# Kernel optimization log

Measured on AMD Instinct MI355X. Metric: run time of the kernel, lower is better.

Reference implementation:

```python
import jax, jax.numpy as jnp
import numpy as np

N = 100000
E = 1600000
F_IN, HID, OUT = 64, 64, 32

def setup_inputs() -> dict:
    key = jax.random.key(0)
    ks = jax.random.split(key, 16)
    s = 0.05
    return {
        "x": jax.random.normal(ks[0], (N, F_IN), jnp.float32),
        "edge_index": jax.random.randint(ks[1], (2, E), 0, N, jnp.int64),
        "edge_attr": jax.random.uniform(ks[2], (E, 1), jnp.float32),
        # distance_processor: Linear(1,16) -> ReLU -> Linear(16,1)
        "Wd1": jax.random.normal(ks[3], (1, 16), jnp.float32) * s,
        "bd1": jnp.zeros((16,), jnp.float32),
        "Wd2": jax.random.normal(ks[4], (16, 1), jnp.float32) * s,
        "bd2": jnp.zeros((1,), jnp.float32),
        # conv1 / conv2 GCN linear weights (in, out) + post-aggregation bias
        "W1c": jax.random.normal(ks[5], (F_IN, HID), jnp.float32) * s,
        "b1c": jnp.zeros((HID,), jnp.float32),
        "W2c": jax.random.normal(ks[6], (HID, HID), jnp.float32) * s,
        "b2c": jnp.zeros((HID,), jnp.float32),
        # output head Linear(hidden, output)
        "Wo": jax.random.normal(ks[7], (HID, OUT), jnp.float32) * s,
        "bo": jnp.zeros((OUT,), jnp.float32),
    }


def _gcn_conv(x, src, dst, ew, W, b, n_nodes):
    """PyG GCNConv with edge weights: add self-loops (weight 1), symmetric norm."""
    h = x @ W                                            # [N, out]
    loop = jnp.arange(n_nodes, dtype=src.dtype)
    src_a = jnp.concatenate([src, loop])                 # [E+N]
    dst_a = jnp.concatenate([dst, loop])
    ew_a = jnp.concatenate([ew, jnp.ones((n_nodes,), ew.dtype)])
    deg = jax.ops.segment_sum(ew_a, dst_a, num_segments=n_nodes)
    dinv = jnp.where(deg > 0, jax.lax.rsqrt(jnp.maximum(deg, 1e-30)), 0.0)
    norm = dinv[src_a] * ew_a * dinv[dst_a]              # [E+N]
    msg = norm[:, None] * h[src_a]                       # gather + scale
    agg = jax.ops.segment_sum(msg, dst_a, num_segments=n_nodes)  # scatter-add
    return agg + b


def reference(x, edge_index, edge_attr, Wd1, bd1, Wd2, bd2, W1c, b1c, W2c, b2c, Wo, bo):
    src, dst = edge_index[0], edge_index[1]
    # edge weight from tiny MLP on distance, squeezed to [E]
    hmlp = jax.nn.relu(edge_attr @ Wd1 + bd1)
    ew = jax.nn.sigmoid(hmlp @ Wd2 + bd2)[:, 0]
    h = jax.nn.relu(_gcn_conv(x, src, dst, ew, W1c, b1c, N))
    # dropout is identity in eval mode
    h = _gcn_conv(h, src, dst, ew, W2c, b2c, N)
    return h @ Wo + bo
```

## Files before the change

### kernel.cpp

```cpp
#include <hip/hip_runtime.h>
#include <math.h>

#define NBMAX 400

__device__ inline ushort f2bf(float f) {
    unsigned u = __float_as_uint(f);
    u += 0x7fff + ((u >> 16) & 1);
    return (ushort)(u >> 16);
}
__device__ inline float bf2f(ushort u) {
    return __uint_as_float(((unsigned)u) << 16);
}

__global__ __launch_bounds__(256) void k_tobf16(const float4* __restrict__ X4,
                                                ushort4* __restrict__ Y4, int n4) {
    int i = blockIdx.x * 256 + threadIdx.x;
    if (i >= n4) return;
    float4 v = X4[i];
    ushort4 o;
    o.x = f2bf(v.x); o.y = f2bf(v.y); o.z = f2bf(v.z); o.w = f2bf(v.w);
    Y4[i] = o;
}

__global__ __launch_bounds__(256) void k_edge3(const float* __restrict__ ea,
                                               const float* __restrict__ Wd1,
                                               const float* __restrict__ bd1,
                                               const float* __restrict__ Wd2,
                                               const float* __restrict__ bd2,
                                               const int* __restrict__ dstv,
                                               float* __restrict__ ew,
                                               int* __restrict__ bcnt,
                                               int E, int chunk) {
    __shared__ float w1[16], b1[16], w2[16];
    __shared__ float b2s;
    __shared__ int lh[NBMAX];
    int tid = threadIdx.x;
    if (tid < 16) {
        w1[tid] = Wd1[tid];
        b1[tid] = bd1[tid];
        w2[tid] = Wd2[tid];
    }
    if (tid == 0) b2s = bd2[0];
    for (int i = tid; i < NBMAX; i += 256) lh[i] = 0;
    __syncthreads();
    int start = blockIdx.x * chunk;
    int end = min(E, start + chunk);
    for (int e = start + tid; e < end; e += 256) {
        float a = ea[e];
        float s = b2s;
#pragma unroll
        for (int j = 0; j < 16; ++j) {
            float h = fmaxf(a * w1[j] + b1[j], 0.0f);
            s += h * w2[j];
        }
        ew[e] = 1.0f / (1.0f + expf(-s));
        atomicAdd(&lh[dstv[e] >> 8], 1);
    }
    __syncthreads();
    for (int i = tid; i < NBMAX; i += 256)
        if (lh[i]) atomicAdd(&bcnt[i], lh[i]);
}

__global__ __launch_bounds__(512) void k_scan_b(const int* __restrict__ bcnt,
                                                int* __restrict__ bbase,
                                                int* __restrict__ bcursor, int nb) {
    __shared__ int s[512];
    int t = threadIdx.x;
    int c = (t < nb) ? bcnt[t] : 0;
    s[t] = c;
    __syncthreads();
    for (int o = 1; o < 512; o <<= 1) {
        int v = (t >= o) ? s[t - o] : 0;
        __syncthreads();
        s[t] += v;
        __syncthreads();
    }
    if (t < nb) {
        int excl = s[t] - c;
        bbase[t] = excl;
        bcursor[t] = excl;
    }
}

__global__ __launch_bounds__(256) void k_scatter(const int* __restrict__ srcv,
                                                 const int* __restrict__ dstv,
                                                 const float* __restrict__ ew,
                                                 int* __restrict__ bcursor,
                                                 int* __restrict__ sdst,
                                                 int* __restrict__ ssrc,
                                                 float* __restrict__ sw,
                                                 int E, int chunk) {
    __shared__ int lh[NBMAX], gb[NBMAX], lc[NBMAX];
    int tid = threadIdx.x;
    for (int i = tid; i < NBMAX; i += 256) { lh[i] = 0; lc[i] = 0; }
    __syncthreads();
    int start = blockIdx.x * chunk;
    int end = min(E, start + chunk);
    for (int e = start + tid; e < end; e += 256)
        atomicAdd(&lh[dstv[e] >> 8], 1);
    __syncthreads();
    for (int i = tid; i < NBMAX; i += 256)
        gb[i] = lh[i] ? atomicAdd(&bcursor[i], lh[i]) : 0;
    __syncthreads();
    for (int e = start + tid; e < end; e += 256) {
        int d = dstv[e];
        int b = d >> 8;
        int p = gb[b] + atomicAdd(&lc[b], 1);
        sdst[p] = d;
        ssrc[p] = srcv[e];
        sw[p] = ew[e];
    }
}

__global__ __launch_bounds__(256) void k_group(const int* __restrict__ sdst,
                                               const int* __restrict__ ssrc,
                                               const float* __restrict__ sw,
                                               const int* __restrict__ bbase,
                                               int2* __restrict__ slots,
                                               int* __restrict__ rowst,
                                               int* __restrict__ cntg,
                                               float* __restrict__ dinv,
                                               int nb, int n, int E) {
    __shared__ int cnt[256], sc[256], ls[256], cur[256];
    __shared__ float dsum[256];
    int b = blockIdx.x;
    int tid = threadIdx.x;
    int r0 = bbase[b];
    int r1 = (b + 1 < nb) ? bbase[b + 1] : E;
    cnt[tid] = 0; cur[tid] = 0; dsum[tid] = 0.0f;
    __syncthreads();
    for (int i = r0 + tid; i < r1; i += 256) {
        int dl = sdst[i] & 255;
        atomicAdd(&cnt[dl], 1);
        atomicAdd(&dsum[dl], sw[i]);
    }
    __syncthreads();
    sc[tid] = cnt[tid];
    __syncthreads();
    for (int o = 1; o < 256; o <<= 1) {
        int v = (tid >= o) ? sc[tid - o] : 0;
        __syncthreads();
        sc[tid] += v;
        __syncthreads();
    }
    ls[tid] = sc[tid] - cnt[tid];
    int dst = (b << 8) + tid;
    if (dst < n) {
        rowst[dst] = r0 + ls[tid];
        cntg[dst] = cnt[tid];
        dinv[dst] = 1.0f / sqrtf(1.0f + dsum[tid]);
    }
    __syncthreads();
    for (int i = r0 + tid; i < r1; i += 256) {
        int dl = sdst[i] & 255;
        int p = r0 + ls[dl] + atomicAdd(&cur[dl], 1);
        slots[p] = make_int2(ssrc[i], __float_as_int(sw[i]));
    }
}

__global__ __launch_bounds__(256) void k_edge2(const float* __restrict__ ea,
                                               const float* __restrict__ Wd1,
                                               const float* __restrict__ bd1,
                                               const float* __restrict__ Wd2,
                                               const float* __restrict__ bd2,
                                               const int* __restrict__ dstv,
                                               float* __restrict__ ew,
                                               int* __restrict__ cnt, int E) {
    __shared__ float w1[16], b1[16], w2[16];
    __shared__ float b2s;
    if (threadIdx.x < 16) {
        w1[threadIdx.x] = Wd1[threadIdx.x];
        b1[threadIdx.x] = bd1[threadIdx.x];
        w2[threadIdx.x] = Wd2[threadIdx.x];
    }
    if (threadIdx.x == 0) b2s = bd2[0];
    __syncthreads();
    int e = blockIdx.x * 256 + threadIdx.x;
    if (e >= E) return;
    float a = ea[e];
    float s = b2s;
#pragma unroll
    for (int j = 0; j < 16; ++j) {
        float h = fmaxf(a * w1[j] + b1[j], 0.0f);
        s += h * w2[j];
    }
    float w = 1.0f / (1.0f + expf(-s));
    ew[e] = w;
    atomicAdd(&cnt[dstv[e]], 1);
}

__global__ __launch_bounds__(256) void k_scan(const int* __restrict__ cnt,
                                              int* __restrict__ rowst,
                                              int* __restrict__ cursor,
                                              int* __restrict__ gcnt, int n) {
    int i = blockIdx.x * 256 + threadIdx.x;
    int lane = threadIdx.x & 63;
    int c = (i < n) ? cnt[i] : 0;
    int pref = c;
#pragma unroll
    for (int o = 1; o < 64; o <<= 1) {
        int t = __shfl_up(pref, o);
        if (lane >= o) pref += t;
    }
    int total = __shfl(pref, 63);
    int base = 0;
    if (lane == 63 && total > 0) base = atomicAdd(gcnt, total);
    base = __shfl(base, 63);
    if (i < n) {
        int start = base + pref - c;
        rowst[i] = start;
        cursor[i] = start;
    }
}

__global__ __launch_bounds__(256) void k_fill2(const int* __restrict__ srcv,
                                               const int* __restrict__ dstv,
                                               const float* __restrict__ ew,
                                               int* __restrict__ cursor,
                                               int2* __restrict__ slots, int E) {
    int e = blockIdx.x * 256 + threadIdx.x;
    if (e >= E) return;
    int p = atomicAdd(&cursor[dstv[e]], 1);
    slots[p] = make_int2(srcv[e], __float_as_int(ew[e]));
}

__global__ __launch_bounds__(256) void k_deg(const int2* __restrict__ slots,
                                             const int* __restrict__ cnt,
                                             const int* __restrict__ rowst,
                                             float* __restrict__ dinv, int n) {
    int t = blockIdx.x * 256 + threadIdx.x;
    int g = t >> 3;
    int sub = t & 7;
    if (g >= n) return;
    int c = cnt[g];
    size_t base = (size_t)rowst[g];
    float s = 0.0f;
    for (int j = sub; j < c; j += 8) s += __int_as_float(slots[base + j].y);
    s += __shfl_xor(s, 1);
    s += __shfl_xor(s, 2);
    s += __shfl_xor(s, 4);
    if (sub == 0) dinv[g] = 1.0f / sqrtf(1.0f + s);
}

__global__ __launch_bounds__(256) void k_agg(const ushort4* __restrict__ Hb,
                                             const int2* __restrict__ slots,
                                             const int* __restrict__ cnt,
                                             const int* __restrict__ rowst,
                                             const float* __restrict__ dinv,
                                             float* __restrict__ Y, int n) {
    float4* Y4 = (float4*)Y;
    int wid = (blockIdx.x * 256 + threadIdx.x) >> 6;
    int lane = threadIdx.x & 63;
    int l = lane & 15;
    int slb = lane & 48;
    int node = wid * 4 + (lane >> 4);
    bool valid = node < n;
    int nc = valid ? node : 0;
    float di = dinv[nc];
    int c = valid ? cnt[nc] : 0;
    size_t base = (size_t)rowst[nc];

    ushort4 h0 = Hb[(size_t)nc * 16 + l];
    float a0 = di * bf2f(h0.x), a1 = di * bf2f(h0.y);
    float a2 = di * bf2f(h0.z), a3 = di * bf2f(h0.w);
    float b0f = 0.f, b1f = 0.f, b2f = 0.f, b3f = 0.f;
    float c0f = 0.f, c1f = 0.f, c2f = 0.f, c3f = 0.f;
    float d0f = 0.f, d1f = 0.f, d2f = 0.f, d3f = 0.f;

    for (int bb = 0; bb < c; bb += 16) {
        int myc = 0;
        float myw = 0.0f;
        if (bb + l < c) {
            int2 pr = slots[base + bb + l];
            myc = pr.x;
            myw = __int_as_float(pr.y) * dinv[myc];
        }
        int mi = min(16, c - bb);
        for (int i = 0; i < mi; i += 4) {
            int n0 = __shfl(myc, slb + i);
            int n1 = __shfl(myc, slb + i + 1);
            int n2 = __shfl(myc, slb + i + 2);
            int n3 = __shfl(myc, slb + i + 3);
            float w0 = __shfl(myw, slb + i);
            float w1 = __shfl(myw, slb + i + 1);
            float w2 = __shfl(myw, slb + i + 2);
            float w3 = __shfl(myw, slb + i + 3);
            ushort4 v0 = Hb[(size_t)n0 * 16 + l];
            ushort4 v1 = Hb[(size_t)n1 * 16 + l];
            ushort4 v2 = Hb[(size_t)n2 * 16 + l];
            ushort4 v3 = Hb[(size_t)n3 * 16 + l];
            a0 += w0 * bf2f(v0.x); a1 += w0 * bf2f(v0.y);
            a2 += w0 * bf2f(v0.z); a3 += w0 * bf2f(v0.w);
            b0f += w1 * bf2f(v1.x); b1f += w1 * bf2f(v1.y);
            b2f += w1 * bf2f(v1.z); b3f += w1 * bf2f(v1.w);
            c0f += w2 * bf2f(v2.x); c1f += w2 * bf2f(v2.y);
            c2f += w2 * bf2f(v2.z); c3f += w2 * bf2f(v2.w);
            d0f += w3 * bf2f(v3.x); d1f += w3 * bf2f(v3.y);
            d2f += w3 * bf2f(v3.z); d3f += w3 * bf2f(v3.w);
        }
    }
    if (valid) {
        float4 o;
        o.x = di * ((a0 + b0f) + (c0f + d0f));
        o.y = di * ((a1 + b1f) + (c1f + d1f));
        o.z = di * ((a2 + b2f) + (c2f + d2f));
        o.w = di * ((a3 + b3f) + (c3f + d3f));
        Y4[(size_t)node * 16 + l] = o;
    }
}

template <int OUTC, bool RELU, bool BF16OUT>
__global__ __launch_bounds__(256) void k_gemm(const float* __restrict__ X,
                                              const float* __restrict__ W,
                                              const float* __restrict__ bias,
                                              void* __restrict__ Yv, int nrows) {
    __shared__ __align__(16) float ws[64 * OUTC];
    __shared__ __align__(16) float xs[64][64];
    int tid = threadIdx.x;
    for (int i = tid; i < 64 * OUTC / 4; i += 256)
        ((float4*)ws)[i] = ((const float4*)W)[i];
    int row0 = blockIdx.x * 64;
    for (int i = tid; i < 64 * 16; i += 256) {
        int r = i >> 4, c4 = i & 15;
        int gr = row0 + r;
        float4 v = make_float4(0.f, 0.f, 0.f, 0.f);
        if (gr < nrows) v = ((const float4*)X)[(size_t)gr * 16 + c4];
        ((float4*)&xs[r][0])[c4] = v;
    }
    __syncthreads();

    int col = tid % OUTC;
    constexpr int RSLOTS = 256 / OUTC;
    constexpr int RPT = 64 / RSLOTS;
    int rs = tid / OUTC;
    float wc[64];
#pragma unroll
    for (int k = 0; k < 64; ++k) wc[k] = ws[k * OUTC + col];
    float bcol = bias[col];

    for (int rr = 0; rr < RPT; ++rr) {
        int r = rs * RPT + rr;
        const float4* x4 = (const float4*)&xs[r][0];
        float acc = 0.0f;
#pragma unroll
        for (int k4 = 0; k4 < 16; ++k4) {
            float4 v = x4[k4];
            acc += v.x * wc[4 * k4 + 0];
            acc += v.y * wc[4 * k4 + 1];
            acc += v.z * wc[4 * k4 + 2];
            acc += v.w * wc[4 * k4 + 3];
        }
        float o = acc + bcol;
        if (RELU) o = fmaxf(o, 0.0f);
        int gr = row0 + r;
        if (gr < nrows) {
            if (BF16OUT) ((ushort*)Yv)[(size_t)gr * OUTC + col] = f2bf(o);
            else         ((float*)Yv)[(size_t)gr * OUTC + col] = o;
        }
    }
}

__global__ __launch_bounds__(256) void k_prepW(const float* __restrict__ W2c,
                                               const float* __restrict__ Wo,
                                               const float* __restrict__ b2c,
                                               const float* __restrict__ bo,
                                               float* __restrict__ W2o,
                                               float* __restrict__ bo2) {
    int t = threadIdx.x;
    for (int idx = t; idx < 64 * 32; idx += 256) {
        int i = idx >> 5, j = idx & 31;
        float s = 0.0f;
        for (int k = 0; k < 64; ++k) s += W2c[i * 64 + k] * Wo[k * 32 + j];
        W2o[idx] = s;
    }
    if (t < 32) {
        float s = bo[t];
        for (int k = 0; k < 64; ++k) s += b2c[k] * Wo[k * 32 + t];
        bo2[t] = s;
    }
}

extern "C" void kernel_launch(void* const* d_in, const int* in_sizes, int n_in,
                              void* d_out, int out_size, void* d_ws, size_t ws_size,
                              hipStream_t stream) {
    const float* x   = (const float*)d_in[0];
    const int*   ei  = (const int*)d_in[1];
    const float* ea  = (const float*)d_in[2];
    const float* Wd1 = (const float*)d_in[3];
    const float* bd1 = (const float*)d_in[4];
    const float* Wd2 = (const float*)d_in[5];
    const float* bd2 = (const float*)d_in[6];
    const float* W1c = (const float*)d_in[7];
    const float* b1c = (const float*)d_in[8];
    const float* W2c = (const float*)d_in[9];
    const float* b2c = (const float*)d_in[10];
    const float* Wo  = (const float*)d_in[11];
    const float* bo  = (const float*)d_in[12];

    const int N = in_sizes[0] / 64;
    const int E = in_sizes[2];
    const int* srcv = ei;
    const int* dstv = ei + E;
    const int NB = (N + 255) >> 8;

    size_t off = 0;
    auto alloc = [&](size_t bytes) -> void* {
        void* p = (char*)d_ws + off;
        off += (bytes + 255) & ~(size_t)255;
        return p;
    };

    int*    cntg  = (int*)   alloc((size_t)N * 4);
    int*    rowst = (int*)   alloc((size_t)N * 4);
    float*  dinv  = (float*) alloc((size_t)N * 4);
    ushort* xb    = (ushort*)alloc((size_t)N * 64 * 2);
    float*  buf1  = (float*) alloc((size_t)N * 64 * 4);
    ushort* buf1b = (ushort*)alloc((size_t)N * 64 * 2);
    float*  W2o   = (float*) alloc(64 * 32 * 4);
    float*  bo2   = (float*) alloc(32 * 4);
    float*  ew    = (float*) alloc((size_t)E * 4);
    int2*   slots = (int2*)  alloc((size_t)E * 8);
    float*  buf2  = buf1;

    const int BA = (N + 15) / 16;
    const int BG = (N + 63) / 64;
    const int BT = (N * 16 + 255) / 256;
    const int GB = 256;
    const int CHUNK = (E + GB - 1) / GB;

    size_t base_need = off;
    size_t sort_need = base_need + 3 * (((size_t)E * 4 + 255) & ~(size_t)255) + 1024;
    const bool fast = ws_size >= sort_need;

    if (fast) {
        int* sdst    = (int*)  alloc((size_t)E * 4);
        int* ssrc    = (int*)  alloc((size_t)E * 4);
        float* sw    = (float*)alloc((size_t)E * 4);
        int* bcnt    = (int*)  alloc(NBMAX * 4);
        int* bbase   = (int*)  alloc(NBMAX * 4);
        int* bcursor = (int*)  alloc(NBMAX * 4);

        hipMemsetAsync(bcnt, 0, NBMAX * 4, stream);
        k_tobf16<<<BT, 256, 0, stream>>>((const float4*)x, (ushort4*)xb, N * 16);
        k_edge3<<<GB, 256, 0, stream>>>(ea, Wd1, bd1, Wd2, bd2, dstv, ew, bcnt,
                                        E, CHUNK);
        k_scan_b<<<1, 512, 0, stream>>>(bcnt, bbase, bcursor, NB);
        k_scatter<<<GB, 256, 0, stream>>>(srcv, dstv, ew, bcursor,
                                          sdst, ssrc, sw, E, CHUNK);
        k_group<<<NB, 256, 0, stream>>>(sdst, ssrc, sw, bbase, slots,
                                        rowst, cntg, dinv, NB, N, E);
        k_prepW<<<1, 256, 0, stream>>>(W2c, Wo, b2c, bo, W2o, bo2);
        k_agg<<<BA, 256, 0, stream>>>((const ushort4*)xb, slots, cntg, rowst,
                                      dinv, buf1, N);
        k_gemm<64, true, true><<<BG, 256, 0, stream>>>(buf1, W1c, b1c, buf1b, N);
        k_agg<<<BA, 256, 0, stream>>>((const ushort4*)buf1b, slots, cntg, rowst,
                                      dinv, buf2, N);
        k_gemm<32, false, false><<<BG, 256, 0, stream>>>(buf2, W2o, bo2, d_out, N);
    } else {
        int* cursor = (int*)alloc((size_t)N * 4);
        int* gcnt   = (int*)alloc(256);
        const int BN = (N + 255) / 256;
        const int BE = (E + 255) / 256;
        const int BD = (N * 8 + 255) / 256;
        hipMemsetAsync(cntg, 0, (size_t)N * 4, stream);
        hipMemsetAsync(gcnt, 0, 4, stream);
        k_tobf16<<<BT, 256, 0, stream>>>((const float4*)x, (ushort4*)xb, N * 16);
        k_edge2<<<BE, 256, 0, stream>>>(ea, Wd1, bd1, Wd2, bd2, dstv, ew, cntg, E);
        k_scan<<<BN, 256, 0, stream>>>(cntg, rowst, cursor, gcnt, N);
        k_fill2<<<BE, 256, 0, stream>>>(srcv, dstv, ew, cursor, slots, E);
        k_deg<<<BD, 256, 0, stream>>>(slots, cntg, rowst, dinv, N);
        k_prepW<<<1, 256, 0, stream>>>(W2c, Wo, b2c, bo, W2o, bo2);
        k_agg<<<BA, 256, 0, stream>>>((const ushort4*)xb, slots, cntg, rowst,
                                      dinv, buf1, N);
        k_gemm<64, true, true><<<BG, 256, 0, stream>>>(buf1, W1c, b1c, buf1b, N);
        k_agg<<<BA, 256, 0, stream>>>((const ushort4*)buf1b, slots, cntg, rowst,
                                      dinv, buf2, N);
        k_gemm<32, false, false><<<BG, 256, 0, stream>>>(buf2, W2o, bo2, d_out, N);
    }
}
```

Before: 329.9 us.

## Move edge MLP into scatter pass and pack sorted edges into int2 with fp16 weight

The edge-weight MLP now runs inside the bucket scatter kernel, so the intermediate ew array is no longer written and then read back. The histogram pass is split into its own light kernel. Each sorted edge is stored as a single int2 holding src, the low 8 bits of dst, and an fp16 weight, replacing three separate arrays. The grid grows from 256 to 512 blocks. Edge weights are rounded to fp16, which lowers precision in both the degree sums and the messages.

New measurement: 312.6 us. -5.3%, faster.

```diff
diff --git a/kernel.cpp b/kernel.cpp
--- a/kernel.cpp
+++ b/kernel.cpp
@@ -1,4 +1,5 @@
 #include <hip/hip_runtime.h>
+#include <hip/hip_fp16.h>
 #include <math.h>
 
 #define NBMAX 400
@@ -22,18 +23,56 @@
     Y4[i] = o;
 }
 
-__global__ __launch_bounds__(256) void k_edge3(const float* __restrict__ ea,
-                                               const float* __restrict__ Wd1,
-                                               const float* __restrict__ bd1,
-                                               const float* __restrict__ Wd2,
-                                               const float* __restrict__ bd2,
-                                               const int* __restrict__ dstv,
-                                               float* __restrict__ ew,
-                                               int* __restrict__ bcnt,
-                                               int E, int chunk) {
+__global__ __launch_bounds__(256) void k_hist(const int* __restrict__ dstv,
+                                              int* __restrict__ bcnt,
+                                              int E, int chunk) {
+    __shared__ int lh[NBMAX];
+    int tid = threadIdx.x;
+    for (int i = tid; i < NBMAX; i += 256) lh[i] = 0;
+    __syncthreads();
+    int start = blockIdx.x * chunk;
+    int end = min(E, start + chunk);
+    for (int e = start + tid; e < end; e += 256)
+        atomicAdd(&lh[dstv[e] >> 8], 1);
+    __syncthreads();
+    for (int i = tid; i < NBMAX; i += 256)
+        if (lh[i]) atomicAdd(&bcnt[i], lh[i]);
+}
+
+__global__ __launch_bounds__(512) void k_scan_b(const int* __restrict__ bcnt,
+                                                int* __restrict__ bbase,
+                                                int* __restrict__ bcursor, int nb) {
+    __shared__ int s[512];
+    int t = threadIdx.x;
+    int c = (t < nb) ? bcnt[t] : 0;
+    s[t] = c;
+    __syncthreads();
+    for (int o = 1; o < 512; o <<= 1) {
+        int v = (t >= o) ? s[t - o] : 0;
+        __syncthreads();
+        s[t] += v;
+        __syncthreads();
+    }
+    if (t < nb) {
+        int excl = s[t] - c;
+        bbase[t] = excl;
+        bcursor[t] = excl;
+    }
+}
+
+__global__ __launch_bounds__(256) void k_edge_scatter(const float* __restrict__ ea,
+                                                      const float* __restrict__ Wd1,
+                                                      const float* __restrict__ bd1,
+                                                      const float* __restrict__ Wd2,
+                                                      const float* __restrict__ bd2,
+                                                      const int* __restrict__ srcv,
+                                                      const int* __restrict__ dstv,
+                                                      int* __restrict__ bcursor,
+                                                      int2* __restrict__ spk,
+                                                      int E, int chunk) {
     __shared__ float w1[16], b1[16], w2[16];
     __shared__ float b2s;
-    __shared__ int lh[NBMAX];
+    __shared__ int lh[NBMAX], gb[NBMAX], lc[NBMAX];
     int tid = threadIdx.x;
     if (tid < 16) {
         w1[tid] = Wd1[tid];
@@ -41,10 +80,16 @@
         w2[tid] = Wd2[tid];
     }
     if (tid == 0) b2s = bd2[0];
-    for (int i = tid; i < NBMAX; i += 256) lh[i] = 0;
+    for (int i = tid; i < NBMAX; i += 256) { lh[i] = 0; lc[i] = 0; }
     __syncthreads();
     int start = blockIdx.x * chunk;
     int end = min(E, start + chunk);
+    for (int e = start + tid; e < end; e += 256)
+        atomicAdd(&lh[dstv[e] >> 8], 1);
+    __syncthreads();
+    for (int i = tid; i < NBMAX; i += 256)
+        gb[i] = lh[i] ? atomicAdd(&bcursor[i], lh[i]) : 0;
+    __syncthreads();
     for (int e = start + tid; e < end; e += 256) {
         float a = ea[e];
         float s = b2s;
@@ -53,68 +98,17 @@
             float h = fmaxf(a * w1[j] + b1[j], 0.0f);
             s += h * w2[j];
         }
-        ew[e] = 1.0f / (1.0f + expf(-s));
-        atomicAdd(&lh[dstv[e] >> 8], 1);
-    }
-    __syncthreads();
-    for (int i = tid; i < NBMAX; i += 256)
-        if (lh[i]) atomicAdd(&bcnt[i], lh[i]);
-}
-
-__global__ __launch_bounds__(512) void k_scan_b(const int* __restrict__ bcnt,
-                                                int* __restrict__ bbase,
-                                                int* __restrict__ bcursor, int nb) {
-    __shared__ int s[512];
-    int t = threadIdx.x;
-    int c = (t < nb) ? bcnt[t] : 0;
-    s[t] = c;
-    __syncthreads();
-    for (int o = 1; o < 512; o <<= 1) {
-        int v = (t >= o) ? s[t - o] : 0;
-        __syncthreads();
-        s[t] += v;
-        __syncthreads();
-    }
-    if (t < nb) {
-        int excl = s[t] - c;
-        bbase[t] = excl;
-        bcursor[t] = excl;
-    }
-}
-
-__global__ __launch_bounds__(256) void k_scatter(const int* __restrict__ srcv,
-                                                 const int* __restrict__ dstv,
-                                                 const float* __restrict__ ew,
-                                                 int* __restrict__ bcursor,
-                                                 int* __restrict__ sdst,
-                                                 int* __restrict__ ssrc,
-                                                 float* __restrict__ sw,
-                                                 int E, int chunk) {
-    __shared__ int lh[NBMAX], gb[NBMAX], lc[NBMAX];
-    int tid = threadIdx.x;
-    for (int i = tid; i < NBMAX; i += 256) { lh[i] = 0; lc[i] = 0; }
-    __syncthreads();
-    int start = blockIdx.x * chunk;
-    int end = min(E, start + chunk);
-    for (int e = start + tid; e < end; e += 256)
-        atomicAdd(&lh[dstv[e] >> 8], 1);
-    __syncthreads();
-    for (int i = tid; i < NBMAX; i += 256)
-        gb[i] = lh[i] ? atomicAdd(&bcursor[i], lh[i]) : 0;
-    __syncthreads();
-    for (int e = start + tid; e < end; e += 256) {
+        float w = 1.0f / (1.0f + expf(-s));
         int d = dstv[e];
         int b = d >> 8;
         int p = gb[b] + atomicAdd(&lc[b], 1);
-        sdst[p] = d;
-        ssrc[p] = srcv[e];
-        sw[p] = ew[e];
-    }
-}
-
-__global__ __launch_bounds__(256) void k_group(const int* __restrict__ sdst,
-                                               const int* __restrict__ ssrc,
-                                               const float* __restrict__ sw,
+        unsigned payload = ((unsigned)(d & 255) << 16) |
+                           (unsigned)__half_as_ushort(__float2half(w));
+        spk[p] = make_int2(srcv[e], (int)payload);
+    }
+}
+
+__global__ __launch_bounds__(256) void k_group(const int2* __restrict__ spk,
                                                const int* __restrict__ bbase,
                                                int2* __restrict__ slots,
                                                int* __restrict__ rowst,
@@ -130,9 +124,10 @@
     cnt[tid] = 0; cur[tid] = 0; dsum[tid] = 0.0f;
     __syncthreads();
     for (int i = r0 + tid; i < r1; i += 256) {
-        int dl = sdst[i] & 255;
+        int2 pr = spk[i];
+        int dl = (pr.y >> 16) & 255;
         atomicAdd(&cnt[dl], 1);
-        atomicAdd(&dsum[dl], sw[i]);
+        atomicAdd(&dsum[dl], __half2float(__ushort_as_half((ushort)(pr.y & 0xffff))));
     }
     __syncthreads();
     sc[tid] = cnt[tid];
@@ -152,9 +147,11 @@
     }
     __syncthreads();
     for (int i = r0 + tid; i < r1; i += 256) {
-        int dl = sdst[i] & 255;
+        int2 pr = spk[i];
+        int dl = (pr.y >> 16) & 255;
+        float wf = __half2float(__ushort_as_half((ushort)(pr.y & 0xffff)));
         int p = r0 + ls[dl] + atomicAdd(&cur[dl], 1);
-        slots[p] = make_int2(ssrc[i], __float_as_int(sw[i]));
+        slots[p] = make_int2(pr.x, __float_as_int(wf));
     }
 }
 
@@ -418,37 +415,33 @@
     ushort* buf1b = (ushort*)alloc((size_t)N * 64 * 2);
     float*  W2o   = (float*) alloc(64 * 32 * 4);
     float*  bo2   = (float*) alloc(32 * 4);
-    float*  ew    = (float*) alloc((size_t)E * 4);
     int2*   slots = (int2*)  alloc((size_t)E * 8);
     float*  buf2  = buf1;
 
     const int BA = (N + 15) / 16;
     const int BG = (N + 63) / 64;
     const int BT = (N * 16 + 255) / 256;
-    const int GB = 256;
+    const int GB = 512;
     const int CHUNK = (E + GB - 1) / GB;
 
     size_t base_need = off;
-    size_t sort_need = base_need + 3 * (((size_t)E * 4 + 255) & ~(size_t)255) + 1024;
+    size_t sort_need = base_need + (((size_t)E * 8 + 255) & ~(size_t)255) + 4096;
     const bool fast = ws_size >= sort_need;
 
     if (fast) {
-        int* sdst    = (int*)  alloc((size_t)E * 4);
-        int* ssrc    = (int*)  alloc((size_t)E * 4);
-        float* sw    = (float*)alloc((size_t)E * 4);
-        int* bcnt    = (int*)  alloc(NBMAX * 4);
-        int* bbase   = (int*)  alloc(NBMAX * 4);
-        int* bcursor = (int*)  alloc(NBMAX * 4);
+        int2* spk    = (int2*)alloc((size_t)E * 8);
+        int* bcnt    = (int*) alloc(NBMAX * 4);
+        int* bbase   = (int*) alloc(NBMAX * 4);
+        int* bcursor = (int*) alloc(NBMAX * 4);
 
         hipMemsetAsync(bcnt, 0, NBMAX * 4, stream);
         k_tobf16<<<BT, 256, 0, stream>>>((const float4*)x, (ushort4*)xb, N * 16);
-        k_edge3<<<GB, 256, 0, stream>>>(ea, Wd1, bd1, Wd2, bd2, dstv, ew, bcnt,
-                                        E, CHUNK);
+        k_hist<<<GB, 256, 0, stream>>>(dstv, bcnt, E, CHUNK);
         k_scan_b<<<1, 512, 0, stream>>>(bcnt, bbase, bcursor, NB);
-        k_scatter<<<GB, 256, 0, stream>>>(srcv, dstv, ew, bcursor,
-                                          sdst, ssrc, sw, E, CHUNK);
-        k_group<<<NB, 256, 0, stream>>>(sdst, ssrc, sw, bbase, slots,
-                                        rowst, cntg, dinv, NB, N, E);
+        k_edge_scatter<<<GB, 256, 0, stream>>>(ea, Wd1, bd1, Wd2, bd2, srcv, dstv,
+                                               bcursor, spk, E, CHUNK);
+        k_group<<<NB, 256, 0, stream>>>(spk, bbase, slots, rowst, cntg, dinv,
+                                        NB, N, E);
         k_prepW<<<1, 256, 0, stream>>>(W2c, Wo, b2c, bo, W2o, bo2);
         k_agg<<<BA, 256, 0, stream>>>((const ushort4*)xb, slots, cntg, rowst,
                                       dinv, buf1, N);
@@ -457,8 +450,9 @@
                                       dinv, buf2, N);
         k_gemm<32, false, false><<<BG, 256, 0, stream>>>(buf2, W2o, bo2, d_out, N);
     } else {
-        int* cursor = (int*)alloc((size_t)N * 4);
-        int* gcnt   = (int*)alloc(256);
+        float* ew   = (float*)alloc((size_t)E * 4);
+        int* cursor = (int*)  alloc((size_t)N * 4);
+        int* gcnt   = (int*)  alloc(256);
         const int BN = (N + 255) / 256;
         const int BE = (E + 255) / 256;
         const int BD = (N * 8 + 255) / 256;
```
